# Kernel tuning notes

Measured on AMD Instinct MI355X. Metric: run time of the kernel, lower is better.

The kernel has to match this reference:

```python
import jax, jax.numpy as jnp
import numpy as np

N, D, FIN, FOUT, H = 50000, 16, 256, 128, 128  # nodes, degree, in/out feat, lstm hidden


def setup_inputs() -> dict:
    key = jax.random.key(0)
    ks = jax.random.split(key, 16)
    E = N * D
    s = 1.0 / np.sqrt(H)
    inp = {
        "in_nodes_features": jax.random.normal(ks[0], (N, FIN), jnp.float32),
        "W_proj": jax.random.normal(ks[1], (FOUT, FIN), jnp.float32) * 0.05,
        "a_src": jax.random.normal(ks[2], (FOUT,), jnp.float32) * 0.1,
        "a_trg": jax.random.normal(ks[3], (FOUT,), jnp.float32) * 0.1,
        "W_skip": jax.random.normal(ks[4], (FOUT, FIN), jnp.float32) * 0.05,
        "bias": jnp.zeros((FOUT,), jnp.float32),
        "w_ih_f": jax.random.uniform(ks[5], (4 * H, FOUT), jnp.float32, -s, s),
        "w_hh_f": jax.random.uniform(ks[6], (4 * H, H), jnp.float32, -s, s),
        "b_ih_f": jax.random.uniform(ks[7], (4 * H,), jnp.float32, -s, s),
        "b_hh_f": jax.random.uniform(ks[8], (4 * H,), jnp.float32, -s, s),
        "w_ih_b": jax.random.uniform(ks[9], (4 * H, FOUT), jnp.float32, -s, s),
        "w_hh_b": jax.random.uniform(ks[10], (4 * H, H), jnp.float32, -s, s),
        "b_ih_b": jax.random.uniform(ks[11], (4 * H,), jnp.float32, -s, s),
        "b_hh_b": jax.random.uniform(ks[12], (4 * H,), jnp.float32, -s, s),
    }
    # uniform-degree graph: each node is target of exactly D edges (sorted by target)
    trg = jnp.repeat(jnp.arange(N, dtype=jnp.int32), D)
    src = jax.random.randint(ks[13], (E,), 0, N, dtype=jnp.int32)
    inp["edge_index"] = jnp.stack([src, trg])  # [2, E]
    return inp


def _lstm_final_h(seq, w_ih, w_hh, b_ih, b_hh):
    # seq: [N, T, F] -> final hidden state [N, H]
    h0 = jnp.zeros((seq.shape[0], w_hh.shape[1]), seq.dtype)
    def step(carry, x_t):
        h, c = carry
        gates = x_t @ w_ih.T + h @ w_hh.T + (b_ih + b_hh)
        i, f, g, o = jnp.split(gates, 4, axis=-1)
        c = jax.nn.sigmoid(f) * c + jax.nn.sigmoid(i) * jnp.tanh(g)
        h = jax.nn.sigmoid(o) * jnp.tanh(c)
        return (h, c), None
    (h, _), _ = jax.lax.scan(step, (h0, h0), jnp.swapaxes(seq, 0, 1))
    return h


def reference(in_nodes_features, W_proj, a_src, a_trg, W_skip, bias,
              w_ih_f, w_hh_f, b_ih_f, b_hh_f, w_ih_b, w_hh_b, b_ih_b, b_hh_b,
              edge_index):
    x = in_nodes_features
    n = x.shape[0]
    src, trg = edge_index[0], edge_index[1]
    proj = x @ W_proj.T                                   # [N, FOUT]
    s_src = proj @ a_src                                  # [N]
    s_trg = proj @ a_trg                                  # [N]
    # lift to edges
    scores = jax.nn.leaky_relu(s_src[src] + s_trg[trg], 0.2)   # [E]
    # neighborhood-aware softmax (global max subtraction as in original)
    e = jnp.exp(scores - jnp.max(scores))
    denom = jax.ops.segment_sum(e, trg, num_segments=n)
    att = e / (denom[trg] + 1e-16)                        # [E]
    weighted = proj[src] * att[:, None]                   # [E, FOUT]
    # trg is sorted with uniform degree: reshape to per-node neighbor sequences
    deg = weighted.shape[0] // n
    att_r = att.reshape(n, deg)
    feat_r = weighted.reshape(n, deg, -1)
    order = jnp.argsort(att_r, axis=1)                    # ascending attention, per node
    seq = jnp.take_along_axis(feat_r, order[:, :, None], axis=1)  # [N, D, FOUT]
    # bidirectional LSTM; hn[-1] == backward-direction final hidden
    out = _lstm_final_h(seq[:, ::-1], w_ih_b, w_hh_b, b_ih_b, b_hh_b)  # [N, H]
    # skip + bias + activation (dims differ -> skip_proj)
    out = out + x @ W_skip.T
    out = out + bias
    return jax.nn.leaky_relu(out, 0.01)
```

## Files before the change

kernel.cpp:

```cpp
#include <hip/hip_runtime.h>
#include <hip/hip_bf16.h>
#include <math.h>

#define N_NODES 50000
#define DEG 16
#define FIN 256
#define FOUT 128
#define HID 128
#define FG 512
#define NEDGE (N_NODES*DEG)
#define NCHUNK (N_NODES/16)
#define NPAIR ((NCHUNK+1)/2)

typedef __bf16 bf16x8 __attribute__((ext_vector_type(8)));
typedef float  f32x4  __attribute__((ext_vector_type(4)));

static __device__ __forceinline__ float u2f(unsigned int u){ union {unsigned int u; float f;} v; v.u=u; return v.f; }
static __device__ __forceinline__ unsigned int f2u(float f){ union {float f; unsigned int u;} v; v.f=f; return v.u; }
static __device__ __forceinline__ unsigned short f2bfu(float f){
  unsigned int u = f2u(f);
  unsigned int r = u + 0x7fffu + ((u >> 16) & 1u);
  return (unsigned short)(r >> 16);
}
static __device__ __forceinline__ float bflo(unsigned int u){ return u2f(u << 16); }
static __device__ __forceinline__ float bfhi(unsigned int u){ return u2f(u & 0xffff0000u); }
static __device__ __forceinline__ float rcpf(float x){ return __builtin_amdgcn_rcpf(x); }
static __device__ __forceinline__ float sigm(float x){ return rcpf(1.f + __expf(-x)); }
static __device__ __forceinline__ float tanhx(float x){ return 1.f - 2.f*rcpf(__expf(2.f*x) + 1.f); }

union FU { bf16x8 bf; unsigned short us[8]; uint4 u4; };

__global__ __launch_bounds__(256) void k_w(
    const float* __restrict__ Wp, const float* __restrict__ Ws,
    const float* __restrict__ wih, const float* __restrict__ a_src, const float* __restrict__ a_trg,
    unsigned short* __restrict__ Wch, unsigned short* __restrict__ Wcl,
    unsigned short* __restrict__ wihh, unsigned short* __restrict__ wihl,
    double* __restrict__ vsrc, double* __restrict__ vtrg,
    unsigned int* __restrict__ gmax_key)
{
  const int b = blockIdx.x, tid = threadIdx.x;
  if (b < 256) {
    const float* src = (b < 128) ? (Wp + b*FIN) : (Ws + (b-128)*FIN);
    const float v = src[tid];
    const unsigned short h = f2bfu(v);
    Wch[b*FIN + tid] = h;
    Wcl[b*FIN + tid] = f2bfu(v - u2f((unsigned)h << 16));
  } else if (b < 512) {
    const int row = (b-256)*2 + (tid >> 7);
    const int k   = tid & 127;
    const float v = wih[row*HID + k];
    const unsigned short h = f2bfu(v);
    wihh[row*HID + k] = h;
    wihl[row*HID + k] = f2bfu(v - u2f((unsigned)h << 16));
  } else {
    if (tid == 0) *gmax_key = 0u;
    const int k = tid;
    double s1 = 0.0, s2 = 0.0;
    for (int i = 0; i < FOUT; ++i) {
      const double w = (double)Wp[i*FIN + k];
      s1 += (double)a_src[i] * w;
      s2 += (double)a_trg[i] * w;
    }
    vsrc[k] = s1; vtrg[k] = s2;
  }
}

__global__ __launch_bounds__(256) void k_s(
    const float* __restrict__ x, const double* __restrict__ vsrc, const double* __restrict__ vtrg,
    double* __restrict__ ssrc, double* __restrict__ strg)
{
  const int n = blockIdx.x*256 + threadIdx.x;
  if (n >= N_NODES) return;
  double ss = 0.0, st = 0.0;
  for (int k = 0; k < FIN; k += 4) {
    const float4 xv = *(const float4*)&x[n*FIN + k];
    ss += xv.x*vsrc[k] + xv.y*vsrc[k+1] + xv.z*vsrc[k+2] + xv.w*vsrc[k+3];
    st += xv.x*vtrg[k] + xv.y*vtrg[k+1] + xv.z*vtrg[k+2] + xv.w*vtrg[k+3];
  }
  ssrc[n] = ss; strg[n] = st;
}

template<int KD, int MODE>
__global__ __launch_bounds__(256) void kgemm(
    const float* __restrict__ Af32,
    const unsigned short* __restrict__ Ah_g, const unsigned short* __restrict__ Al_g,
    const unsigned short* __restrict__ Bh_g, const unsigned short* __restrict__ Bl_g,
    const float* __restrict__ bias, float* __restrict__ outf,
    unsigned short* __restrict__ o_h, unsigned short* __restrict__ o_l)
{
  __shared__ unsigned short At[2][128*64];
  __shared__ unsigned short Bt[2][64*64];
  const int tid = threadIdx.x;
  const int bm = blockIdx.x, bn = blockIdx.y;
  const int r0 = bm*128;
  const int wave = tid >> 6, lane = tid & 63, c = lane & 15, q = lane >> 4;
  const int srow = tid >> 3, sg = tid & 7;

  f32x4 acc[2][4];
  #pragma unroll
  for (int rt = 0; rt < 2; ++rt)
    #pragma unroll
    for (int ct = 0; ct < 4; ++ct) acc[rt][ct] = (f32x4){0.f,0.f,0.f,0.f};

  for (int kt = 0; kt < KD/64; ++kt) {
    const int k0 = kt*64;
    __syncthreads();
    #pragma unroll
    for (int rr = 0; rr < 4; ++rr) {
      const int row = rr*32 + srow;
      int grow = r0 + row; if (grow >= N_NODES) grow = N_NODES-1;
      const int ga = grow*KD + k0 + sg*8;
      const int la = row*64 + (((sg ^ (row & 7))) << 3);
      if (MODE == 0) {
        const float4 v0 = *(const float4*)&Af32[ga];
        const float4 v1 = *(const float4*)&Af32[ga + 4];
        union { unsigned short us[8]; uint4 u4; } H, L;
        H.us[0]=f2bfu(v0.x); L.us[0]=f2bfu(v0.x - u2f((unsigned)H.us[0] << 16));
        H.us[1]=f2bfu(v0.y); L.us[1]=f2bfu(v0.y - u2f((unsigned)H.us[1] << 16));
        H.us[2]=f2bfu(v0.z); L.us[2]=f2bfu(v0.z - u2f((unsigned)H.us[2] << 16));
        H.us[3]=f2bfu(v0.w); L.us[3]=f2bfu(v0.w - u2f((unsigned)H.us[3] << 16));
        H.us[4]=f2bfu(v1.x); L.us[4]=f2bfu(v1.x - u2f((unsigned)H.us[4] << 16));
        H.us[5]=f2bfu(v1.y); L.us[5]=f2bfu(v1.y - u2f((unsigned)H.us[5] << 16));
        H.us[6]=f2bfu(v1.z); L.us[6]=f2bfu(v1.z - u2f((unsigned)H.us[6] << 16));
        H.us[7]=f2bfu(v1.w); L.us[7]=f2bfu(v1.w - u2f((unsigned)H.us[7] << 16));
        *(uint4*)&At[0][la] = H.u4;
        *(uint4*)&At[1][la] = L.u4;
      } else {
        *(uint4*)&At[0][la] = *(const uint4*)&Ah_g[ga];
        *(uint4*)&At[1][la] = *(const uint4*)&Al_g[ga];
      }
    }
    #pragma unroll
    for (int rr = 0; rr < 2; ++rr) {
      const int row = rr*32 + srow;
      int wr;
      if (MODE == 0) wr = bn*64 + row;
      else { const int j = bn*64 + row; wr = (j & 3)*HID + (j >> 2); }
      const int ga = wr*KD + k0 + sg*8;
      const int la = row*64 + (((sg ^ (row & 7))) << 3);
      *(uint4*)&Bt[0][la] = *(const uint4*)&Bh_g[ga];
      *(uint4*)&Bt[1][la] = *(const uint4*)&Bl_g[ga];
    }
    __syncthreads();

    #pragma unroll
    for (int s = 0; s < 2; ++s) {
      FU Af[2][2], Bf[4][2];
      #pragma unroll
      for (int rt = 0; rt < 2; ++rt) {
        const int row = wave*32 + rt*16 + c;
        const int ad = row*64 + (((((s<<2)+q) ^ (row & 7))) << 3);
        Af[rt][0].u4 = *(const uint4*)&At[0][ad];
        Af[rt][1].u4 = *(const uint4*)&At[1][ad];
      }
      #pragma unroll
      for (int ct = 0; ct < 4; ++ct) {
        const int row = ct*16 + c;
        const int ad = row*64 + (((((s<<2)+q) ^ (row & 7))) << 3);
        Bf[ct][0].u4 = *(const uint4*)&Bt[0][ad];
        Bf[ct][1].u4 = *(const uint4*)&Bt[1][ad];
      }
      #pragma unroll
      for (int rt = 0; rt < 2; ++rt)
        #pragma unroll
        for (int ct = 0; ct < 4; ++ct) {
          acc[rt][ct] = __builtin_amdgcn_mfma_f32_16x16x32_bf16(Af[rt][0].bf, Bf[ct][0].bf, acc[rt][ct], 0,0,0);
          acc[rt][ct] = __builtin_amdgcn_mfma_f32_16x16x32_bf16(Af[rt][1].bf, Bf[ct][0].bf, acc[rt][ct], 0,0,0);
          acc[rt][ct] = __builtin_amdgcn_mfma_f32_16x16x32_bf16(Af[rt][0].bf, Bf[ct][1].bf, acc[rt][ct], 0,0,0);
        }
    }
  }
  __syncthreads();

  if (MODE == 0 && bn >= 2) {
    #pragma unroll
    for (int ct = 0; ct < 4; ++ct) {
      const int col = bn*64 + ct*16 + c - 128;
      const float bv = bias[col];
      #pragma unroll
      for (int rt = 0; rt < 2; ++rt)
        #pragma unroll
        for (int i = 0; i < 4; ++i) {
          const int row = r0 + wave*32 + rt*16 + q*4 + i;
          if (row < N_NODES) outf[row*FOUT + col] = acc[rt][ct][i] + bv;
        }
    }
  } else {
    #pragma unroll
    for (int rt = 0; rt < 2; ++rt)
      #pragma unroll
      for (int ct = 0; ct < 4; ++ct)
        #pragma unroll
        for (int i = 0; i < 4; ++i) {
          const int lrow = wave*32 + rt*16 + q*4 + i;
          const int lcol = ct*16 + c;
          const float v = acc[rt][ct][i];
          const unsigned short h = f2bfu(v);
          At[0][lrow*64 + lcol] = h;
          if (MODE == 0) At[1][lrow*64 + lcol] = f2bfu(v - u2f((unsigned)h << 16));
        }
    __syncthreads();
    const int ncols = (MODE == 0) ? FOUT : FG;
    #pragma unroll
    for (int rr = 0; rr < 4; ++rr) {
      const int row = rr*32 + srow;
      const int grow = r0 + row;
      if (grow < N_NODES) {
        const int dst = grow*ncols + bn*64 + sg*8;
        *(uint4*)&o_h[dst] = *(const uint4*)&At[0][row*64 + sg*8];
        if (MODE == 0) *(uint4*)&o_l[dst] = *(const uint4*)&At[1][row*64 + sg*8];
      }
    }
  }
}

__global__ __launch_bounds__(256) void k3_scores(
    const double* __restrict__ ssrc, const double* __restrict__ strg,
    const int* __restrict__ esrc, const int* __restrict__ etrg,
    double* __restrict__ scod, unsigned int* __restrict__ gmax_key)
{
  const int n = blockIdx.x*256 + threadIdx.x;
  float lmax = -3.0e38f;
  if (n < N_NODES) {
    const double stn = strg[etrg[n*DEG]];
    #pragma unroll
    for (int j = 0; j < DEG; ++j) {
      const int e = n*DEG + j;
      double sc = ssrc[esrc[e]] + stn;
      sc = (sc > 0.0) ? sc : 0.2*sc;
      scod[e] = sc;
      lmax = fmaxf(lmax, (float)sc);
    }
  }
  #pragma unroll
  for (int off = 32; off > 0; off >>= 1)
    lmax = fmaxf(lmax, __shfl_down(lmax, off, 64));
  __shared__ float wmax[4];
  if ((threadIdx.x & 63) == 0) wmax[threadIdx.x >> 6] = lmax;
  __syncthreads();
  if (threadIdx.x == 0) {
    const float mv = fmaxf(fmaxf(wmax[0], wmax[1]), fmaxf(wmax[2], wmax[3]));
    const unsigned int u = f2u(mv);
    const unsigned int key = (u & 0x80000000u) ? ~u : (u | 0x80000000u);
    atomicMax(gmax_key, key);
  }
}

__global__ __launch_bounds__(256) void k4_att(
    const double* __restrict__ scod, const int* __restrict__ esrc,
    const unsigned int* __restrict__ gmax_key,
    float* __restrict__ atts, int* __restrict__ srcs)
{
  const int n = blockIdx.x*256 + threadIdx.x;
  if (n >= N_NODES) return;
  const unsigned int key = *gmax_key;
  const unsigned int u = (key & 0x80000000u) ? (key ^ 0x80000000u) : ~key;
  const float gmax = u2f(u);

  double sc[DEG]; float av[DEG]; int si[DEG];
  float sum = 0.f;
  #pragma unroll
  for (int j = 0; j < DEG; ++j) {
    sc[j] = scod[n*DEG + j];
    av[j] = __expf((float)sc[j] - gmax);
    sum  += av[j];
    si[j] = esrc[n*DEG + j];
  }
  const float inv = 1.f/(sum + 1e-16f);
  #pragma unroll
  for (int j = 0; j < DEG; ++j) {
    int r = 0;
    #pragma unroll
    for (int k = 0; k < DEG; ++k)
      r += (sc[k] > sc[j]) || (sc[k] == sc[j] && k > j);
    atts[n*DEG + r] = av[j]*inv;
    srcs[n*DEG + r] = si[j];
  }
}

__global__ __launch_bounds__(1024) void k5_lstm(
    const __hip_bfloat16* __restrict__ G, const float* __restrict__ whh,
    const float* __restrict__ bih, const float* __restrict__ bhh,
    const float* __restrict__ atts, const int* __restrict__ srcs,
    float* __restrict__ out)
{
  __shared__ unsigned short Bs[32768];
  __shared__ unsigned short hbuf[2][2][16*128];
  __shared__ float attb[2][16][16];
  __shared__ int   srcb[2][16][16];

  const int tid  = threadIdx.x;
  const int wave = tid >> 6;
  const int team = wave >> 3;
  const int w8   = wave & 7;
  const int lane = tid & 63;
  const int c    = lane & 15;
  const int q    = lane >> 4;
  const int fcol = w8*16 + c;
  const int nb0  = q*4;
  const int ttid = tid & 511;

  #pragma unroll
  for (int j = 0; j < 4; ++j) {
    const int s   = tid + j*1024;
    const int sg_ = s >> 11, skt = (s >> 9) & 3, sw8 = (s >> 6) & 7, sl = s & 63;
    const float* p = whh + (((sg_ + 2)*128 + sw8*16 + (sl & 15))*128 + skt*32 + (sl >> 4)*8);
    const float4 v0 = *(const float4*)p;
    const float4 v1 = *(const float4*)(p + 4);
    union { unsigned short us[8]; uint4 u4; } P;
    P.us[0]=f2bfu(v0.x); P.us[1]=f2bfu(v0.y); P.us[2]=f2bfu(v0.z); P.us[3]=f2bfu(v0.w);
    P.us[4]=f2bfu(v1.x); P.us[5]=f2bfu(v1.y); P.us[6]=f2bfu(v1.z); P.us[7]=f2bfu(v1.w);
    *(uint4*)&Bs[s*8] = P.u4;
  }

  FU Brg[2][4];
  #pragma unroll
  for (int g = 0; g < 2; ++g) {
    const float* wr = whh + (g*HID + fcol)*HID + q*8;
    #pragma unroll
    for (int kt = 0; kt < 4; ++kt) {
      const float4 w0 = *(const float4*)(wr + kt*32);
      const float4 w1 = *(const float4*)(wr + kt*32 + 4);
      Brg[g][kt].us[0]=f2bfu(w0.x); Brg[g][kt].us[1]=f2bfu(w0.y);
      Brg[g][kt].us[2]=f2bfu(w0.z); Brg[g][kt].us[3]=f2bfu(w0.w);
      Brg[g][kt].us[4]=f2bfu(w1.x); Brg[g][kt].us[5]=f2bfu(w1.y);
      Brg[g][kt].us[6]=f2bfu(w1.z); Brg[g][kt].us[7]=f2bfu(w1.w);
    }
  }

  float bsum[4];
  #pragma unroll
  for (int g = 0; g < 4; ++g) bsum[g] = bih[g*HID + fcol] + bhh[g*HID + fcol];

  int aoff[4];
  #pragma unroll
  for (int kt = 0; kt < 4; ++kt)
    aoff[kt] = c*128 + (((kt*4 + q) ^ c) & 15)*8;

  const unsigned short* Gu = (const unsigned short*)G;

  for (int pair = blockIdx.x; pair < NPAIR; pair += gridDim.x) {
    int chunk = pair*2 + team;
    const bool act = (chunk < NCHUNK);
    if (!act) chunk = NCHUNK - 1;
    const int nb = chunk * 16;
    __syncthreads();
    if (ttid < 256) {
      ((float*)attb[team])[ttid] = atts[nb*DEG + ttid];
      ((int*)  srcb[team])[ttid] = srcs[nb*DEG + ttid];
    }
    __syncthreads();

    float cst[4] = {0.f,0.f,0.f,0.f};
    float hv[4]  = {0.f,0.f,0.f,0.f};
    uint2 pf[4];
    #pragma unroll
    for (int r = 0; r < 4; ++r) {
      const int s = srcb[team][nb0 + r][0];
      pf[r] = *(const uint2*)(Gu + (size_t)s*FG + fcol*4);
    }

    #pragma unroll 4
    for (int t = 0; t < DEG; ++t) {
      uint2 cur[4]; float at[4];
      #pragma unroll
      for (int r = 0; r < 4; ++r) { cur[r] = pf[r]; at[r] = attb[team][nb0 + r][t]; }
      if (t < DEG-1) {
        #pragma unroll
        for (int r = 0; r < 4; ++r) {
          const int s = srcb[team][nb0 + r][t+1];
          pf[r] = *(const uint2*)(Gu + (size_t)s*FG + fcol*4);
        }
      }
      f32x4 acc[4];
      #pragma unroll
      for (int r = 0; r < 4; ++r) {
        acc[0][r] = bsum[0] + at[r]*bflo(cur[r].x);
        acc[1][r] = bsum[1] + at[r]*bfhi(cur[r].x);
        acc[2][r] = bsum[2] + at[r]*bflo(cur[r].y);
        acc[3][r] = bsum[3] + at[r]*bfhi(cur[r].y);
      }
      if (t > 0) {
        __syncthreads();
        const unsigned short* hb = hbuf[team][(t-1) & 1];
        FU A[4];
        #pragma unroll
        for (int kt = 0; kt < 4; ++kt) A[kt].u4 = *(const uint4*)(hb + aoff[kt]);
        #pragma unroll
        for (int g = 0; g < 2; ++g) {
          #pragma unroll
          for (int kt = 0; kt < 4; ++kt)
            acc[g] = __builtin_amdgcn_mfma_f32_16x16x32_bf16(A[kt].bf, Brg[g][kt].bf, acc[g], 0, 0, 0);
        }
        #pragma unroll
        for (int g = 2; g < 4; ++g) {
          FU Bf[4];
          #pragma unroll
          for (int kt = 0; kt < 4; ++kt)
            Bf[kt].u4 = *(const uint4*)&Bs[((((g-2)*4 + kt)*8 + w8)*64 + lane)*8];
          #pragma unroll
          for (int kt = 0; kt < 4; ++kt)
            acc[g] = __builtin_amdgcn_mfma_f32_16x16x32_bf16(A[kt].bf, Bf[kt].bf, acc[g], 0, 0, 0);
        }
      }
      #pragma unroll
      for (int r = 0; r < 4; ++r) {
        const float ig = sigm (acc[0][r]);
        const float fg = sigm (acc[1][r]);
        const float gg = tanhx(acc[2][r]);
        const float og = sigm (acc[3][r]);
        cst[r] = fg*cst[r] + ig*gg;
        hv[r]  = og*tanhx(cst[r]);
      }
      if (t < DEG-1) {
        unsigned short* hw = hbuf[team][t & 1];
        #pragma unroll
        for (int r = 0; r < 4; ++r) {
          const float other = __shfl_xor(hv[r], 1, 64);
          if ((c & 1) == 0) {
            const unsigned pack = (unsigned)f2bfu(hv[r]) | ((unsigned)f2bfu(other) << 16);
            const int node = nb0 + r;
            const int k = fcol;
            const int half = node*128 + (((k >> 3) ^ node) & 15)*8 + (k & 7);
            *(unsigned*)(hw + half) = pack;
          }
        }
      }
    }
    if (act) {
      #pragma unroll
      for (int r = 0; r < 4; ++r) {
        const int node = nb + nb0 + r;
        const float v = hv[r] + out[node*HID + fcol];
        out[node*HID + fcol] = (v > 0.f) ? v : 0.01f*v;
      }
    }
  }
}

extern "C" void kernel_launch(void* const* d_in, const int* in_sizes, int n_in,
                              void* d_out, int out_size, void* d_ws, size_t ws_size,
                              hipStream_t stream)
{
  (void)in_sizes; (void)n_in; (void)out_size; (void)ws_size;
  const float* x     = (const float*)d_in[0];
  const float* Wp    = (const float*)d_in[1];
  const float* a_src = (const float*)d_in[2];
  const float* a_trg = (const float*)d_in[3];
  const float* Ws    = (const float*)d_in[4];
  const float* bias  = (const float*)d_in[5];
  const float* wih_b = (const float*)d_in[10];
  const float* whh_b = (const float*)d_in[11];
  const float* bih_b = (const float*)d_in[12];
  const float* bhh_b = (const float*)d_in[13];
  const int*   eidx  = (const int*)d_in[14];
  const int* esrc = eidx;
  const int* etrg = eidx + NEDGE;
  float* out = (float*)d_out;

  unsigned char* ws = (unsigned char*)d_ws;
  unsigned int*   gmax = (unsigned int*)(ws + 0);
  unsigned short* Gh   = (unsigned short*)(ws + 256);
  unsigned short* projh= (unsigned short*)(ws + 51200256);
  unsigned short* projl= (unsigned short*)(ws + 64000256);
  double*         scod = (double*)(ws + 51200256);
  float*          atts = (float*) (ws + 64000256);
  int*            srcs = (int*)   (ws + 67200256);
  unsigned short* Wch  = (unsigned short*)(ws + 76800256);
  unsigned short* Wcl  = (unsigned short*)(ws + 76931328);
  unsigned short* wihh = (unsigned short*)(ws + 77062400);
  unsigned short* wihl = (unsigned short*)(ws + 77193472);
  double*         vsrc = (double*)(ws + 77324544);
  double*         vtrg = (double*)(ws + 77326592);
  double*         ssrc = (double*)(ws + 77328640);
  double*         strg = (double*)(ws + 77728640);

  k_w<<<dim3(513), dim3(256), 0, stream>>>(Wp, Ws, wih_b, a_src, a_trg,
                                           Wch, Wcl, wihh, wihl, vsrc, vtrg, gmax);
  k_s<<<dim3((N_NODES+255)/256), dim3(256), 0, stream>>>(x, vsrc, vtrg, ssrc, strg);
  kgemm<FIN,0><<<dim3((N_NODES+127)/128, 4), dim3(256), 0, stream>>>(
      x, (const unsigned short*)0, (const unsigned short*)0, Wch, Wcl, bias, out, projh, projl);
  kgemm<HID,1><<<dim3((N_NODES+127)/128, 8), dim3(256), 0, stream>>>(
      (const float*)0, projh, projl, wihh, wihl, bias, out, Gh, (unsigned short*)0);
  k3_scores<<<dim3((N_NODES+255)/256), dim3(256), 0, stream>>>(ssrc, strg, esrc, etrg, scod, gmax);
  k4_att<<<dim3((N_NODES+255)/256), dim3(256), 0, stream>>>(scod, esrc, gmax, atts, srcs);
  k5_lstm<<<dim3(256), dim3(1024), 0, stream>>>((const __hip_bfloat16*)Gh, whh_b, bih_b, bhh_b, atts, srcs, out);
}
```

Measured before the change: 501.6 us.

## Split LSTM kernel into single-team 512-thread blocks with larger grid

The LSTM recurrence kernel previously ran two 8-wave teams per 1024-thread block, so both teams shared every per-timestep __syncthreads. Each block now holds one team of 512 threads, and the grid doubles to 512 blocks. Barriers therefore only cover the waves that actually share the hidden state. Each block reloads the recurrent weights into LDS, which doubles that preload traffic, and LDS use per block (~68KB for the weight buffer) may still cap how many blocks fit per CU despite the launch-bounds hint.

```diff
diff --git a/kernel.cpp b/kernel.cpp
--- a/kernel.cpp
+++ b/kernel.cpp
@@ -10,7 +10,7 @@
 #define FG 512
 #define NEDGE (N_NODES*DEG)
 #define NCHUNK (N_NODES/16)
-#define NPAIR ((NCHUNK+1)/2)
+#define K5GRID 512
 
 typedef __bf16 bf16x8 __attribute__((ext_vector_type(8)));
 typedef float  f32x4  __attribute__((ext_vector_type(4)));
@@ -278,31 +278,28 @@
   }
 }
 
-__global__ __launch_bounds__(1024) void k5_lstm(
+__global__ __launch_bounds__(512, 4) void k5_lstm(
     const __hip_bfloat16* __restrict__ G, const float* __restrict__ whh,
     const float* __restrict__ bih, const float* __restrict__ bhh,
     const float* __restrict__ atts, const int* __restrict__ srcs,
     float* __restrict__ out)
 {
   __shared__ unsigned short Bs[32768];
-  __shared__ unsigned short hbuf[2][2][16*128];
-  __shared__ float attb[2][16][16];
-  __shared__ int   srcb[2][16][16];
+  __shared__ unsigned short hbuf[2][16*128];
+  __shared__ float attb[16][16];
+  __shared__ int   srcb[16][16];
 
   const int tid  = threadIdx.x;
   const int wave = tid >> 6;
-  const int team = wave >> 3;
-  const int w8   = wave & 7;
   const int lane = tid & 63;
   const int c    = lane & 15;
   const int q    = lane >> 4;
-  const int fcol = w8*16 + c;
+  const int fcol = wave*16 + c;
   const int nb0  = q*4;
-  const int ttid = tid & 511;
-
-  #pragma unroll
-  for (int j = 0; j < 4; ++j) {
-    const int s   = tid + j*1024;
+
+  #pragma unroll
+  for (int j = 0; j < 8; ++j) {
+    const int s   = tid + j*512;
     const int sg_ = s >> 11, skt = (s >> 9) & 3, sw8 = (s >> 6) & 7, sl = s & 63;
     const float* p = whh + (((sg_ + 2)*128 + sw8*16 + (sl & 15))*128 + skt*32 + (sl >> 4)*8);
     const float4 v0 = *(const float4*)p;
@@ -339,15 +336,12 @@
 
   const unsigned short* Gu = (const unsigned short*)G;
 
-  for (int pair = blockIdx.x; pair < NPAIR; pair += gridDim.x) {
-    int chunk = pair*2 + team;
-    const bool act = (chunk < NCHUNK);
-    if (!act) chunk = NCHUNK - 1;
+  for (int chunk = blockIdx.x; chunk < NCHUNK; chunk += K5GRID) {
     const int nb = chunk * 16;
     __syncthreads();
-    if (ttid < 256) {
-      ((float*)attb[team])[ttid] = atts[nb*DEG + ttid];
-      ((int*)  srcb[team])[ttid] = srcs[nb*DEG + ttid];
+    if (tid < 256) {
+      ((float*)attb)[tid] = atts[nb*DEG + tid];
+      ((int*)  srcb)[tid] = srcs[nb*DEG + tid];
     }
     __syncthreads();
 
@@ -356,7 +350,7 @@
     uint2 pf[4];
     #pragma unroll
     for (int r = 0; r < 4; ++r) {
-      const int s = srcb[team][nb0 + r][0];
+      const int s = srcb[nb0 + r][0];
       pf[r] = *(const uint2*)(Gu + (size_t)s*FG + fcol*4);
     }
 
@@ -364,11 +358,11 @@
     for (int t = 0; t < DEG; ++t) {
       uint2 cur[4]; float at[4];
       #pragma unroll
-      for (int r = 0; r < 4; ++r) { cur[r] = pf[r]; at[r] = attb[team][nb0 + r][t]; }
+      for (int r = 0; r < 4; ++r) { cur[r] = pf[r]; at[r] = attb[nb0 + r][t]; }
       if (t < DEG-1) {
         #pragma unroll
         for (int r = 0; r < 4; ++r) {
-          const int s = srcb[team][nb0 + r][t+1];
+          const int s = srcb[nb0 + r][t+1];
           pf[r] = *(const uint2*)(Gu + (size_t)s*FG + fcol*4);
         }
       }
@@ -382,7 +376,7 @@
       }
       if (t > 0) {
         __syncthreads();
-        const unsigned short* hb = hbuf[team][(t-1) & 1];
+        const unsigned short* hb = hbuf[(t-1) & 1];
         FU A[4];
         #pragma unroll
         for (int kt = 0; kt < 4; ++kt) A[kt].u4 = *(const uint4*)(hb + aoff[kt]);
@@ -397,7 +391,7 @@
           FU Bf[4];
           #pragma unroll
           for (int kt = 0; kt < 4; ++kt)
-            Bf[kt].u4 = *(const uint4*)&Bs[((((g-2)*4 + kt)*8 + w8)*64 + lane)*8];
+            Bf[kt].u4 = *(const uint4*)&Bs[((((g-2)*4 + kt)*8 + wave)*64 + lane)*8];
           #pragma unroll
           for (int kt = 0; kt < 4; ++kt)
             acc[g] = __builtin_amdgcn_mfma_f32_16x16x32_bf16(A[kt].bf, Bf[kt].bf, acc[g], 0, 0, 0);
@@ -413,7 +407,7 @@
         hv[r]  = og*tanhx(cst[r]);
       }
       if (t < DEG-1) {
-        unsigned short* hw = hbuf[team][t & 1];
+        unsigned short* hw = hbuf[t & 1];
         #pragma unroll
         for (int r = 0; r < 4; ++r) {
           const float other = __shfl_xor(hv[r], 1, 64);
@@ -427,13 +421,11 @@
         }
       }
     }
-    if (act) {
-      #pragma unroll
-      for (int r = 0; r < 4; ++r) {
-        const int node = nb + nb0 + r;
-        const float v = hv[r] + out[node*HID + fcol];
-        out[node*HID + fcol] = (v > 0.f) ? v : 0.01f*v;
-      }
+    #pragma unroll
+    for (int r = 0; r < 4; ++r) {
+      const int node = nb + nb0 + r;
+      const float v = hv[r] + out[node*HID + fcol];
+      out[node*HID + fcol] = (v > 0.f) ? v : 0.01f*v;
     }
   }
 }
@@ -484,5 +476,5 @@
       (const float*)0, projh, projl, wihh, wihl, bias, out, Gh, (unsigned short*)0);
   k3_scores<<<dim3((N_NODES+255)/256), dim3(256), 0, stream>>>(ssrc, strg, esrc, etrg, scod, gmax);
   k4_att<<<dim3((N_NODES+255)/256), dim3(256), 0, stream>>>(scod, esrc, gmax, atts, srcs);
-  k5_lstm<<<dim3(256), dim3(1024), 0, stream>>>((const __hip_bfloat16*)Gh, whh_b, bih_b, bhh_b, atts, srcs, out);
-}
+  k5_lstm<<<dim3(K5GRID), dim3(512), 0, stream>>>((const __hip_bfloat16*)Gh, whh_b, bih_b, bhh_b, atts, srcs, out);
+}
```

New measurement: 505.6 us. No clear change (+0.8%).
